# Kernel optimization log

Hardware: AMD Instinct MI355X
Metric: run time of the kernel (lower is better)

## Reference

```python
import jax, jax.numpy as jnp
import numpy as np

SIZE = 128
N_ATOMS = 100000
N_BONDS = 400000
N_PAIRS = 400000
N_ANGLES = 800000
LN_EPS = 1e-5


def _layernorm(h, w, b):
    m = jnp.mean(h, axis=-1, keepdims=True)
    v = jnp.mean(jnp.square(h - m), axis=-1, keepdims=True)
    return (h - m) * jax.lax.rsqrt(v + LN_EPS) * w + b


def _forward(x, bond_x, sc_pair_x, angles,
             W_bm, W_sc, W1, b1, W2, b2,
             ln1_w, ln1_b, ln2_w, ln2_b,
             bond_idx, sc_idx, angles_idx):
    n_atoms = x.shape[0]
    n_bonds = bond_x.shape[0]

    # ---- sublayer 1: bond message passing ----
    h = _layernorm(x, ln1_w, ln1_b)                       # [n_atoms, d]
    # aggregate angle features onto bonds
    bond_ang = jax.ops.segment_sum(angles, angles_idx, num_segments=n_bonds)
    src, dst = bond_idx[:, 0], bond_idx[:, 1]
    msg = jax.nn.relu((h[src] + bond_x + bond_ang) @ W_bm)  # [n_bonds, d]
    agg = jax.ops.segment_sum(msg, dst, num_segments=n_atoms)
    x = x + (agg @ W1 + b1)                               # residual (dropout=0)

    # ---- sublayer 2: scalar-coupling pair message passing ----
    h2 = _layernorm(x, ln2_w, ln2_b)
    i, j = sc_idx[:, 0], sc_idx[:, 1]
    msg2 = jax.nn.relu((h2[i] + h2[j] + sc_pair_x) @ W_sc)  # [n_pairs, d]
    agg2 = jax.ops.segment_sum(msg2, i, num_segments=n_atoms)
    return x + (agg2 @ W2 + b2)


def setup_inputs() -> dict:
    key = jax.random.key(0)
    ks = jax.random.split(key, 16)
    s = 1.0 / np.sqrt(SIZE)
    inp = {
        "x": jax.random.normal(ks[0], (N_ATOMS, SIZE), jnp.float32),
        "bond_x": jax.random.normal(ks[1], (N_BONDS, SIZE), jnp.float32),
        "sc_pair_x": jax.random.normal(ks[2], (N_PAIRS, SIZE), jnp.float32),
        "angles": jax.random.normal(ks[3], (N_ANGLES, SIZE), jnp.float32),
        "W_bm": jax.random.normal(ks[4], (SIZE, SIZE), jnp.float32) * s,
        "W_sc": jax.random.normal(ks[5], (SIZE, SIZE), jnp.float32) * s,
        "W1": jax.random.normal(ks[6], (SIZE, SIZE), jnp.float32) * s,
        "b1": jnp.zeros((SIZE,), jnp.float32),
        "W2": jax.random.normal(ks[7], (SIZE, SIZE), jnp.float32) * s,
        "b2": jnp.zeros((SIZE,), jnp.float32),
        "ln1_w": jax.random.uniform(ks[8], (SIZE,), jnp.float32),
        "ln1_b": jnp.zeros((SIZE,), jnp.float32),
        "ln2_w": jax.random.uniform(ks[9], (SIZE,), jnp.float32),
        "ln2_b": jnp.zeros((SIZE,), jnp.float32),
        "mask": jnp.ones((N_ATOMS,), jnp.bool_),
        "bond_idx": jax.random.randint(ks[10], (N_BONDS, 2), 0, N_ATOMS),
        "sc_idx": jax.random.randint(ks[11], (N_PAIRS, 2), 0, N_ATOMS),
        "angles_idx": jax.random.randint(ks[12], (N_ANGLES,), 0, N_BONDS),
    }
    return inp


def reference(x, bond_x, sc_pair_x, angles, W_bm, W_sc, W1, b1, W2, b2,
              ln1_w, ln1_b, ln2_w, ln2_b, mask, bond_idx, sc_idx, angles_idx):
    # mask is in the torch forward signature but unused in its body
    return _forward(x, bond_x, sc_pair_x, angles, W_bm, W_sc, W1, b1, W2, b2,
                    ln1_w, ln1_b, ln2_w, ln2_b, bond_idx, sc_idx, angles_idx)
```

## Files before the change

### kernel.cpp

```cpp
#include <hip/hip_runtime.h>

#define SZ 128
#define NATOMS 100000
#define NBONDS 400000
#define NPAIRS 400000
#define NANG   800000

typedef float f32x4 __attribute__((ext_vector_type(4)));
typedef short s16x8 __attribute__((ext_vector_type(8)));

__device__ __forceinline__ unsigned short f2bf(float f) {
  union { float f; unsigned u; } v; v.f = f;
  unsigned r = v.u + 0x7FFFu + ((v.u >> 16) & 1u);
  return (unsigned short)(r >> 16);
}
__device__ __forceinline__ float bf2f(unsigned short h) {
  union { unsigned u; float f; } v; v.u = ((unsigned)h) << 16;
  return v.f;
}

#define AGG_OFF      0ull
#define AGG2_OFF     51200000ull
#define CNT_OFF      102400000ull
#define FILL_OFF     104000000ull
#define ZERO_BYTES   105600000ull
#define START_OFF    105600000ull
#define ALIST_OFF    107200000ull
#define BSUM_OFF     110400000ull
#define H_OFF        110404096ull
#define H2_OFF       136004096ull
#define WT_BM_OFF    161604096ull
#define WT_SC_OFF    (WT_BM_OFF + 32768ull)
#define WT1_OFF      (WT_SC_OFF + 32768ull)
#define WT2_OFF      (WT1_OFF + 32768ull)

#define SCAN_EPB 1024
#define NSCAN_BLOCKS ((NBONDS + SCAN_EPB - 1) / SCAN_EPB)

__global__ __launch_bounds__(256) void k_prep_w(const float* __restrict__ W,
                                                s16x8* __restrict__ Wt) {
  int cid = blockIdx.x * 256 + threadIdx.x;
  int nt8 = cid >> 8, kk = (cid >> 6) & 3, l = cid & 63;
  int col = nt8 * 16 + (l & 15);
  int k0  = kk * 32 + (l >> 4) * 8;
  s16x8 v;
#pragma unroll
  for (int i = 0; i < 8; ++i) v[i] = (short)f2bf(W[(k0 + i) * SZ + col]);
  Wt[cid] = v;
}

__global__ __launch_bounds__(256) void k_ln(const float* __restrict__ x,
                                            const float* __restrict__ g,
                                            const float* __restrict__ bvec,
                                            unsigned short* __restrict__ hout) {
  int row  = blockIdx.x * 4 + (threadIdx.x >> 6);
  int lane = threadIdx.x & 63;
  float2 v = *(const float2*)(x + (size_t)row * SZ + lane * 2);
  float s = v.x + v.y, sq = v.x * v.x + v.y * v.y;
#pragma unroll
  for (int off = 32; off; off >>= 1) { s += __shfl_xor(s, off); sq += __shfl_xor(sq, off); }
  float m = s * 0.0078125f;
  float var = sq * 0.0078125f - m * m;
  float rstd = rsqrtf(var + 1e-5f);
  float2 gv = *(const float2*)(g + lane * 2);
  float2 bv = *(const float2*)(bvec + lane * 2);
  float y0 = (v.x - m) * rstd * gv.x + bv.x;
  float y1 = (v.y - m) * rstd * gv.y + bv.y;
  unsigned pack = (unsigned)f2bf(y0) | ((unsigned)f2bf(y1) << 16);
  ((unsigned*)hout)[(size_t)row * 64 + lane] = pack;
}

__global__ __launch_bounds__(256) void k_hist(const int* __restrict__ aidx,
                                              int* __restrict__ cnt) {
  int id = blockIdx.x * 256 + threadIdx.x;
  if (id < NANG) atomicAdd(&cnt[aidx[id]], 1);
}

__global__ __launch_bounds__(256) void k_scan1(const int* __restrict__ cnt,
                                               int* __restrict__ start,
                                               int* __restrict__ bsum) {
  __shared__ int wsum[4];
  int tid = threadIdx.x, bid = blockIdx.x;
  int base = bid * SCAN_EPB + tid * 4;
  int4 c;
  if (base + 3 < NBONDS) {
    c = *(const int4*)(cnt + base);
  } else {
    c.x = (base + 0 < NBONDS) ? cnt[base + 0] : 0;
    c.y = (base + 1 < NBONDS) ? cnt[base + 1] : 0;
    c.z = (base + 2 < NBONDS) ? cnt[base + 2] : 0;
    c.w = (base + 3 < NBONDS) ? cnt[base + 3] : 0;
  }
  int tsum = c.x + c.y + c.z + c.w;
  int lane = tid & 63, wid = tid >> 6;
  int inc = tsum;
#pragma unroll
  for (int off = 1; off < 64; off <<= 1) {
    int o = __shfl_up(inc, off);
    if (lane >= off) inc += o;
  }
  if (lane == 63) wsum[wid] = inc;
  __syncthreads();
  int woff = 0;
#pragma unroll
  for (int wq = 0; wq < 4; ++wq) { if (wq < wid) woff += wsum[wq]; }
  int s0 = woff + inc - tsum;
  if (base + 0 < NBONDS) { start[base + 0] = s0; } s0 += c.x;
  if (base + 1 < NBONDS) { start[base + 1] = s0; } s0 += c.y;
  if (base + 2 < NBONDS) { start[base + 2] = s0; } s0 += c.z;
  if (base + 3 < NBONDS) { start[base + 3] = s0; }
  if (tid == 255) {
    int tot = 0;
#pragma unroll
    for (int wq = 0; wq < 4; ++wq) tot += wsum[wq];
    bsum[bid] = tot;
  }
}

__global__ __launch_bounds__(512) void k_scan2(int* __restrict__ bsum, int n) {
  __shared__ int tmp[2][512];
  int tid = threadIdx.x;
  tmp[0][tid] = (tid < n) ? bsum[tid] : 0;
  int pi = 0;
  for (int off = 1; off < 512; off <<= 1) {
    __syncthreads();
    int t = tmp[pi][tid];
    if (tid >= off) t += tmp[pi][tid - off];
    tmp[pi ^ 1][tid] = t;
    pi ^= 1;
  }
  __syncthreads();
  if (tid < n) bsum[tid] = (tid == 0) ? 0 : tmp[pi][tid - 1];
}

__global__ __launch_bounds__(256) void k_scan_add(int* __restrict__ start,
                                                  const int* __restrict__ bsum) {
  int id = blockIdx.x * 256 + threadIdx.x;
  if (id < NBONDS) start[id] += bsum[id / SCAN_EPB];
}

__global__ __launch_bounds__(256) void k_fill(const int* __restrict__ aidx,
                                              const int* __restrict__ start,
                                              int* __restrict__ fill,
                                              int* __restrict__ alist) {
  int id = blockIdx.x * 256 + threadIdx.x;
  if (id < NANG) {
    int b = aidx[id];
    int p = atomicAdd(&fill[b], 1);
    alist[start[b] + p] = id;
  }
}

__global__ __launch_bounds__(256, 4) void k_msg1(const unsigned short* __restrict__ h,
                                                 const float* __restrict__ bx,
                                                 const float* __restrict__ angles,
                                                 const int* __restrict__ start,
                                                 const int* __restrict__ cnt,
                                                 const int* __restrict__ alist,
                                                 const int* __restrict__ bidx,
                                                 const s16x8* __restrict__ Wt,
                                                 float* __restrict__ agg) {
  __shared__ s16x8 Wl[2048];
  int tid = threadIdx.x;
  for (int i = tid; i < 2048; i += 256) Wl[i] = Wt[i];
  __syncthreads();
  int w = tid >> 6, l = tid & 63;
  int grp = l >> 4;
  int rl  = l & 15;
  int gw = blockIdx.x * 4 + w;
  int nw = gridDim.x * 4;
  for (int tile = gw; tile < NBONDS / 16; tile += nw) {
    int base = tile * 16;
    int b = base + rl;
    int s = bidx[2 * b];
    int s0 = start[b], nc = cnt[b];
    int aj[4] = {0, 0, 0, 0};
#pragma unroll
    for (int t = 0; t < 4; ++t) {
      if (t < nc) aj[t] = alist[s0 + t];
    }
    f32x4 acc[8];
#pragma unroll
    for (int nb = 0; nb < 8; ++nb) acc[nb] = (f32x4){0.f, 0.f, 0.f, 0.f};
#pragma unroll
    for (int kk = 0; kk < 4; ++kk) {
      const int co = kk * 32 + grp * 8;
      uint4 hv = *(const uint4*)(h + (size_t)s * SZ + co);
      float4 b0 = *(const float4*)(bx + (size_t)b * SZ + co);
      float4 b1 = *(const float4*)(bx + (size_t)b * SZ + co + 4);
      float a[8];
      a[0] = b0.x; a[1] = b0.y; a[2] = b0.z; a[3] = b0.w;
      a[4] = b1.x; a[5] = b1.y; a[6] = b1.z; a[7] = b1.w;
#pragma unroll
      for (int t = 0; t < 4; ++t) {
        if (t < nc) {
          const float* ap = angles + (size_t)aj[t] * SZ + co;
          float4 u0 = *(const float4*)ap;
          float4 u1 = *(const float4*)(ap + 4);
          a[0] += u0.x; a[1] += u0.y; a[2] += u0.z; a[3] += u0.w;
          a[4] += u1.x; a[5] += u1.y; a[6] += u1.z; a[7] += u1.w;
        }
      }
      for (int t = 4; t < nc; ++t) {
        int ar = alist[s0 + t];
        const float* ap = angles + (size_t)ar * SZ + co;
        float4 u0 = *(const float4*)ap;
        float4 u1 = *(const float4*)(ap + 4);
        a[0] += u0.x; a[1] += u0.y; a[2] += u0.z; a[3] += u0.w;
        a[4] += u1.x; a[5] += u1.y; a[6] += u1.z; a[7] += u1.w;
      }
      const unsigned short* hp = (const unsigned short*)&hv;
      s16x8 af;
#pragma unroll
      for (int i = 0; i < 8; ++i) af[i] = (short)f2bf(bf2f(hp[i]) + a[i]);
#pragma unroll
      for (int nb = 0; nb < 8; ++nb)
        acc[nb] = __builtin_amdgcn_mfma_f32_16x16x32_bf16(af, Wl[(nb * 4 + kk) * 64 + l], acc[nb], 0, 0, 0);
    }
#pragma unroll
    for (int p = 0; p < 4; ++p) {
      int row = base + grp * 4 + p;
      int d = bidx[2 * row + 1];
      float* pb = agg + (size_t)d * SZ + rl;
#pragma unroll
      for (int nb = 0; nb < 8; ++nb)
        unsafeAtomicAdd(pb + nb * 16, fmaxf(acc[nb][p], 0.f));
    }
  }
}

__global__ __launch_bounds__(256, 4) void k_msg2(const unsigned short* __restrict__ h2,
                                                 const float* __restrict__ scp,
                                                 const int* __restrict__ sidx,
                                                 const s16x8* __restrict__ Wt,
                                                 float* __restrict__ agg2) {
  __shared__ s16x8 Wl[2048];
  int tid = threadIdx.x;
  for (int i = tid; i < 2048; i += 256) Wl[i] = Wt[i];
  __syncthreads();
  int w = tid >> 6, l = tid & 63;
  int grp = l >> 4;
  int rl  = l & 15;
  int gw = blockIdx.x * 4 + w;
  int nw = gridDim.x * 4;
  for (int tile = gw; tile < NPAIRS / 16; tile += nw) {
    int base = tile * 16;
    int b = base + rl;
    int i0 = sidx[2 * b], j0 = sidx[2 * b + 1];
    f32x4 acc[8];
#pragma unroll
    for (int nb = 0; nb < 8; ++nb) acc[nb] = (f32x4){0.f, 0.f, 0.f, 0.f};
#pragma unroll
    for (int kk = 0; kk < 4; ++kk) {
      const int co = kk * 32 + grp * 8;
      uint4 hv1 = *(const uint4*)(h2 + (size_t)i0 * SZ + co);
      uint4 hv2 = *(const uint4*)(h2 + (size_t)j0 * SZ + co);
      float4 s0v = *(const float4*)(scp + (size_t)b * SZ + co);
      float4 s1v = *(const float4*)(scp + (size_t)b * SZ + co + 4);
      const unsigned short* p1 = (const unsigned short*)&hv1;
      const unsigned short* p2 = (const unsigned short*)&hv2;
      float a[8];
      a[0] = s0v.x; a[1] = s0v.y; a[2] = s0v.z; a[3] = s0v.w;
      a[4] = s1v.x; a[5] = s1v.y; a[6] = s1v.z; a[7] = s1v.w;
      s16x8 af;
#pragma unroll
      for (int i = 0; i < 8; ++i) af[i] = (short)f2bf(bf2f(p1[i]) + bf2f(p2[i]) + a[i]);
#pragma unroll
      for (int nb = 0; nb < 8; ++nb)
        acc[nb] = __builtin_amdgcn_mfma_f32_16x16x32_bf16(af, Wl[(nb * 4 + kk) * 64 + l], acc[nb], 0, 0, 0);
    }
#pragma unroll
    for (int p = 0; p < 4; ++p) {
      int row = base + grp * 4 + p;
      int d = sidx[2 * row];
      float* pb = agg2 + (size_t)d * SZ + rl;
#pragma unroll
      for (int nb = 0; nb < 8; ++nb)
        unsafeAtomicAdd(pb + nb * 16, fmaxf(acc[nb][p], 0.f));
    }
  }
}

__global__ __launch_bounds__(256) void k_update1(const float* __restrict__ agg,
                                                 const float* __restrict__ x,
                                                 const float* __restrict__ b1,
                                                 const float* __restrict__ lnw,
                                                 const float* __restrict__ lnb,
                                                 const s16x8* __restrict__ Wt,
                                                 float* __restrict__ out,
                                                 unsigned short* __restrict__ h2) {
  __shared__ s16x8 Wl[2048];
  __shared__ s16x8 Tl[256];
  __shared__ float Xl[16][128];
  int tid = threadIdx.x;
  for (int i = tid; i < 2048; i += 256) Wl[i] = Wt[i];
  __syncthreads();
  int r = tid >> 4, kc = tid & 15;
  int w = tid >> 6, l = tid & 63;
  int colb = w * 32 + (l & 15);
  int rowb = (l >> 4) * 4;
  float bb0 = b1[colb], bb1 = b1[colb + 16];
  float2 g2 = *(const float2*)(lnw + l * 2);
  float2 be2 = *(const float2*)(lnb + l * 2);
  for (int tile = blockIdx.x; tile < NATOMS / 16; tile += gridDim.x) {
    int base = tile * 16;
    int a = base + r;
    float qb[8];
    *(float4*)&qb[0] = *(const float4*)(agg + (size_t)a * SZ + kc * 8);
    *(float4*)&qb[4] = *(const float4*)(agg + (size_t)a * SZ + kc * 8 + 4);
    s16x8 tv;
#pragma unroll
    for (int i = 0; i < 8; ++i) tv[i] = (short)f2bf(qb[i]);
    Tl[(kc >> 2) * 64 + (kc & 3) * 16 + r] = tv;
    __syncthreads();
    f32x4 acc0 = {0.f, 0.f, 0.f, 0.f}, acc1 = {0.f, 0.f, 0.f, 0.f};
#pragma unroll
    for (int kk = 0; kk < 4; ++kk) {
      s16x8 av = Tl[kk * 64 + l];
      acc0 = __builtin_amdgcn_mfma_f32_16x16x32_bf16(av, Wl[((w * 2 + 0) * 4 + kk) * 64 + l], acc0, 0, 0, 0);
      acc1 = __builtin_amdgcn_mfma_f32_16x16x32_bf16(av, Wl[((w * 2 + 1) * 4 + kk) * 64 + l], acc1, 0, 0, 0);
    }
#pragma unroll
    for (int p = 0; p < 4; ++p) {
      int atom = base + rowb + p;
      float v0 = acc0[p] + bb0 + x[(size_t)atom * SZ + colb];
      float v1 = acc1[p] + bb1 + x[(size_t)atom * SZ + colb + 16];
      out[(size_t)atom * SZ + colb] = v0;
      out[(size_t)atom * SZ + colb + 16] = v1;
      Xl[rowb + p][colb] = v0;
      Xl[rowb + p][colb + 16] = v1;
    }
    __syncthreads();
#pragma unroll
    for (int rr = 0; rr < 4; ++rr) {
      int rw = w * 4 + rr;
      float2 v = *(const float2*)&Xl[rw][l * 2];
      float s = v.x + v.y, sq = v.x * v.x + v.y * v.y;
#pragma unroll
      for (int off = 32; off; off >>= 1) { s += __shfl_xor(s, off); sq += __shfl_xor(sq, off); }
      float m = s * 0.0078125f;
      float var = sq * 0.0078125f - m * m;
      float rstd = rsqrtf(var + 1e-5f);
      float y0 = (v.x - m) * rstd * g2.x + be2.x;
      float y1 = (v.y - m) * rstd * g2.y + be2.y;
      unsigned pack = (unsigned)f2bf(y0) | ((unsigned)f2bf(y1) << 16);
      ((unsigned*)h2)[(size_t)(base + rw) * 64 + l] = pack;
    }
    __syncthreads();
  }
}

__global__ __launch_bounds__(256) void k_update2(const float* __restrict__ agg2,
                                                 const float* __restrict__ b2,
                                                 const s16x8* __restrict__ Wt,
                                                 float* __restrict__ out) {
  __shared__ s16x8 Wl[2048];
  __shared__ s16x8 Tl[256];
  int tid = threadIdx.x;
  for (int i = tid; i < 2048; i += 256) Wl[i] = Wt[i];
  __syncthreads();
  int r = tid >> 4, kc = tid & 15;
  int w = tid >> 6, l = tid & 63;
  int colb = w * 32 + (l & 15);
  int rowb = (l >> 4) * 4;
  float bb0 = b2[colb], bb1 = b2[colb + 16];
  for (int tile = blockIdx.x; tile < NATOMS / 16; tile += gridDim.x) {
    int base = tile * 16;
    int a = base + r;
    float qb[8];
    *(float4*)&qb[0] = *(const float4*)(agg2 + (size_t)a * SZ + kc * 8);
    *(float4*)&qb[4] = *(const float4*)(agg2 + (size_t)a * SZ + kc * 8 + 4);
    s16x8 tv;
#pragma unroll
    for (int i = 0; i < 8; ++i) tv[i] = (short)f2bf(qb[i]);
    Tl[(kc >> 2) * 64 + (kc & 3) * 16 + r] = tv;
    __syncthreads();
    f32x4 acc0 = {0.f, 0.f, 0.f, 0.f}, acc1 = {0.f, 0.f, 0.f, 0.f};
#pragma unroll
    for (int kk = 0; kk < 4; ++kk) {
      s16x8 av = Tl[kk * 64 + l];
      acc0 = __builtin_amdgcn_mfma_f32_16x16x32_bf16(av, Wl[((w * 2 + 0) * 4 + kk) * 64 + l], acc0, 0, 0, 0);
      acc1 = __builtin_amdgcn_mfma_f32_16x16x32_bf16(av, Wl[((w * 2 + 1) * 4 + kk) * 64 + l], acc1, 0, 0, 0);
    }
#pragma unroll
    for (int p = 0; p < 4; ++p) {
      int atom = base + rowb + p;
      out[(size_t)atom * SZ + colb]      += acc0[p] + bb0;
      out[(size_t)atom * SZ + colb + 16] += acc1[p] + bb1;
    }
    __syncthreads();
  }
}

extern "C" void kernel_launch(void* const* d_in, const int* in_sizes, int n_in,
                              void* d_out, int out_size, void* d_ws, size_t ws_size,
                              hipStream_t stream) {
  (void)in_sizes; (void)n_in; (void)out_size; (void)ws_size;
  const float* x        = (const float*)d_in[0];
  const float* bond_x   = (const float*)d_in[1];
  const float* sc_pair  = (const float*)d_in[2];
  const float* angles   = (const float*)d_in[3];
  const float* W_bm     = (const float*)d_in[4];
  const float* W_sc     = (const float*)d_in[5];
  const float* W1       = (const float*)d_in[6];
  const float* b1       = (const float*)d_in[7];
  const float* W2       = (const float*)d_in[8];
  const float* b2       = (const float*)d_in[9];
  const float* ln1w     = (const float*)d_in[10];
  const float* ln1b     = (const float*)d_in[11];
  const float* ln2w     = (const float*)d_in[12];
  const float* ln2b     = (const float*)d_in[13];
  const int* bond_idx   = (const int*)d_in[15];
  const int* sc_idx     = (const int*)d_in[16];
  const int* ang_idx    = (const int*)d_in[17];
  float* out = (float*)d_out;
  char* ws = (char*)d_ws;

  float* agg      = (float*)(ws + AGG_OFF);
  float* agg2     = (float*)(ws + AGG2_OFF);
  int*   cnt      = (int*)(ws + CNT_OFF);
  int*   fill     = (int*)(ws + FILL_OFF);
  int*   start    = (int*)(ws + START_OFF);
  int*   alist    = (int*)(ws + ALIST_OFF);
  int*   bsum     = (int*)(ws + BSUM_OFF);
  unsigned short* hbuf  = (unsigned short*)(ws + H_OFF);
  unsigned short* h2buf = (unsigned short*)(ws + H2_OFF);
  s16x8* wt_bm = (s16x8*)(ws + WT_BM_OFF);
  s16x8* wt_sc = (s16x8*)(ws + WT_SC_OFF);
  s16x8* wt1   = (s16x8*)(ws + WT1_OFF);
  s16x8* wt2   = (s16x8*)(ws + WT2_OFF);

  hipMemsetAsync(ws, 0, ZERO_BYTES, stream);

  k_prep_w<<<8, 256, 0, stream>>>(W_bm, wt_bm);
  k_prep_w<<<8, 256, 0, stream>>>(W_sc, wt_sc);
  k_prep_w<<<8, 256, 0, stream>>>(W1, wt1);
  k_prep_w<<<8, 256, 0, stream>>>(W2, wt2);

  k_hist<<<(NANG + 255) / 256, 256, 0, stream>>>(ang_idx, cnt);
  k_scan1<<<NSCAN_BLOCKS, 256, 0, stream>>>(cnt, start, bsum);
  k_scan2<<<1, 512, 0, stream>>>(bsum, NSCAN_BLOCKS);
  k_scan_add<<<(NBONDS + 255) / 256, 256, 0, stream>>>(start, bsum);
  k_fill<<<(NANG + 255) / 256, 256, 0, stream>>>(ang_idx, start, fill, alist);

  k_ln<<<NATOMS / 4, 256, 0, stream>>>(x, ln1w, ln1b, hbuf);
  k_msg1<<<2048, 256, 0, stream>>>(hbuf, bond_x, angles, start, cnt, alist, bond_idx, wt_bm, agg);
  k_update1<<<1024, 256, 0, stream>>>(agg, x, b1, ln2w, ln2b, wt1, out, h2buf);
  k_msg2<<<2048, 256, 0, stream>>>(h2buf, sc_pair, sc_idx, wt_sc, agg2);
  k_update2<<<1024, 256, 0, stream>>>(agg2, b2, wt2, out);
}
```

Measured before the change: 795.0 us.

## Sort bonds and pairs by destination atom and merge same-target atomics

Builds counting-sort permutations of bonds (by destination atom) and pairs (by source atom i), then processes edges in that sorted order in the message kernels. Consecutive rows with the same destination are summed in registers before a single atomic add, which cuts the number of global float atomics and improves their locality. In exchange it adds ten extra small prep kernels and makes the bond_x and sc_pair_x row gathers indirect, so those reads are no longer contiguous. With random indices and about four edges per atom, adjacent rows in a group of four often share a destination.

```diff
diff --git a/kernel.cpp b/kernel.cpp
--- a/kernel.cpp
+++ b/kernel.cpp
@@ -23,19 +23,30 @@
 #define AGG2_OFF     51200000ull
 #define CNT_OFF      102400000ull
 #define FILL_OFF     104000000ull
-#define ZERO_BYTES   105600000ull
-#define START_OFF    105600000ull
-#define ALIST_OFF    107200000ull
-#define BSUM_OFF     110400000ull
-#define H_OFF        110404096ull
-#define H2_OFF       136004096ull
-#define WT_BM_OFF    161604096ull
+#define CNTB_OFF     105600000ull
+#define FILLB_OFF    106000000ull
+#define CNTP_OFF     106400000ull
+#define FILLP_OFF    106800000ull
+#define ZERO_BYTES   107200000ull
+#define START_OFF    107200000ull
+#define ALIST_OFF    108800000ull
+#define BSUM_OFF     112000000ull
+#define STARTB_OFF   112004096ull
+#define BLIST_OFF    112404096ull
+#define DLIST_OFF    114004096ull
+#define BSUMB_OFF    115604096ull
+#define STARTP_OFF   115608192ull
+#define PLIST_OFF    116008192ull
+#define ILIST_OFF    117608192ull
+#define BSUMP_OFF    119208192ull
+#define H_OFF        119212288ull
+#define H2_OFF       144812288ull
+#define WT_BM_OFF    170412288ull
 #define WT_SC_OFF    (WT_BM_OFF + 32768ull)
 #define WT1_OFF      (WT_SC_OFF + 32768ull)
 #define WT2_OFF      (WT1_OFF + 32768ull)
 
 #define SCAN_EPB 1024
-#define NSCAN_BLOCKS ((NBONDS + SCAN_EPB - 1) / SCAN_EPB)
 
 __global__ __launch_bounds__(256) void k_prep_w(const float* __restrict__ W,
                                                 s16x8* __restrict__ Wt) {
@@ -70,26 +81,27 @@
   ((unsigned*)hout)[(size_t)row * 64 + lane] = pack;
 }
 
-__global__ __launch_bounds__(256) void k_hist(const int* __restrict__ aidx,
+__global__ __launch_bounds__(256) void k_hist(const int* __restrict__ idx, int n,
+                                              int stride, int off,
                                               int* __restrict__ cnt) {
   int id = blockIdx.x * 256 + threadIdx.x;
-  if (id < NANG) atomicAdd(&cnt[aidx[id]], 1);
+  if (id < n) atomicAdd(&cnt[idx[id * stride + off]], 1);
 }
 
 __global__ __launch_bounds__(256) void k_scan1(const int* __restrict__ cnt,
                                                int* __restrict__ start,
-                                               int* __restrict__ bsum) {
+                                               int* __restrict__ bsum, int N) {
   __shared__ int wsum[4];
   int tid = threadIdx.x, bid = blockIdx.x;
   int base = bid * SCAN_EPB + tid * 4;
   int4 c;
-  if (base + 3 < NBONDS) {
+  if (base + 3 < N) {
     c = *(const int4*)(cnt + base);
   } else {
-    c.x = (base + 0 < NBONDS) ? cnt[base + 0] : 0;
-    c.y = (base + 1 < NBONDS) ? cnt[base + 1] : 0;
-    c.z = (base + 2 < NBONDS) ? cnt[base + 2] : 0;
-    c.w = (base + 3 < NBONDS) ? cnt[base + 3] : 0;
+    c.x = (base + 0 < N) ? cnt[base + 0] : 0;
+    c.y = (base + 1 < N) ? cnt[base + 1] : 0;
+    c.z = (base + 2 < N) ? cnt[base + 2] : 0;
+    c.w = (base + 3 < N) ? cnt[base + 3] : 0;
   }
   int tsum = c.x + c.y + c.z + c.w;
   int lane = tid & 63, wid = tid >> 6;
@@ -105,10 +117,10 @@
 #pragma unroll
   for (int wq = 0; wq < 4; ++wq) { if (wq < wid) woff += wsum[wq]; }
   int s0 = woff + inc - tsum;
-  if (base + 0 < NBONDS) { start[base + 0] = s0; } s0 += c.x;
-  if (base + 1 < NBONDS) { start[base + 1] = s0; } s0 += c.y;
-  if (base + 2 < NBONDS) { start[base + 2] = s0; } s0 += c.z;
-  if (base + 3 < NBONDS) { start[base + 3] = s0; }
+  if (base + 0 < N) { start[base + 0] = s0; } s0 += c.x;
+  if (base + 1 < N) { start[base + 1] = s0; } s0 += c.y;
+  if (base + 2 < N) { start[base + 2] = s0; } s0 += c.z;
+  if (base + 3 < N) { start[base + 3] = s0; }
   if (tid == 255) {
     int tot = 0;
 #pragma unroll
@@ -134,20 +146,24 @@
 }
 
 __global__ __launch_bounds__(256) void k_scan_add(int* __restrict__ start,
-                                                  const int* __restrict__ bsum) {
+                                                  const int* __restrict__ bsum, int N) {
   int id = blockIdx.x * 256 + threadIdx.x;
-  if (id < NBONDS) start[id] += bsum[id / SCAN_EPB];
-}
-
-__global__ __launch_bounds__(256) void k_fill(const int* __restrict__ aidx,
+  if (id < N) start[id] += bsum[id / SCAN_EPB];
+}
+
+__global__ __launch_bounds__(256) void k_fill(const int* __restrict__ idx, int n,
+                                              int stride, int off,
                                               const int* __restrict__ start,
                                               int* __restrict__ fill,
-                                              int* __restrict__ alist) {
+                                              int* __restrict__ list,
+                                              int* __restrict__ klist) {
   int id = blockIdx.x * 256 + threadIdx.x;
-  if (id < NANG) {
-    int b = aidx[id];
-    int p = atomicAdd(&fill[b], 1);
-    alist[start[b] + p] = id;
+  if (id < n) {
+    int k = idx[id * stride + off];
+    int p = atomicAdd(&fill[k], 1);
+    int pos = start[k] + p;
+    list[pos] = id;
+    if (klist) klist[pos] = k;
   }
 }
 
@@ -158,6 +174,8 @@
                                                  const int* __restrict__ cnt,
                                                  const int* __restrict__ alist,
                                                  const int* __restrict__ bidx,
+                                                 const int* __restrict__ blist,
+                                                 const int* __restrict__ dlist,
                                                  const s16x8* __restrict__ Wt,
                                                  float* __restrict__ agg) {
   __shared__ s16x8 Wl[2048];
@@ -171,7 +189,7 @@
   int nw = gridDim.x * 4;
   for (int tile = gw; tile < NBONDS / 16; tile += nw) {
     int base = tile * 16;
-    int b = base + rl;
+    int b = blist[base + rl];
     int s = bidx[2 * b];
     int s0 = start[b], nc = cnt[b];
     int aj[4] = {0, 0, 0, 0};
@@ -217,21 +235,37 @@
       for (int nb = 0; nb < 8; ++nb)
         acc[nb] = __builtin_amdgcn_mfma_f32_16x16x32_bf16(af, Wl[(nb * 4 + kk) * 64 + l], acc[nb], 0, 0, 0);
     }
-#pragma unroll
-    for (int p = 0; p < 4; ++p) {
-      int row = base + grp * 4 + p;
-      int d = bidx[2 * row + 1];
-      float* pb = agg + (size_t)d * SZ + rl;
-#pragma unroll
-      for (int nb = 0; nb < 8; ++nb)
-        unsafeAtomicAdd(pb + nb * 16, fmaxf(acc[nb][p], 0.f));
-    }
+    int4 dv = *(const int4*)(dlist + base + grp * 4);
+    int dn[4] = {dv.x, dv.y, dv.z, dv.w};
+    float v[8];
+#pragma unroll
+    for (int nb = 0; nb < 8; ++nb) v[nb] = fmaxf(acc[nb][0], 0.f);
+    int dprev = dn[0];
+#pragma unroll
+    for (int p = 1; p < 4; ++p) {
+      if (dn[p] == dprev) {
+#pragma unroll
+        for (int nb = 0; nb < 8; ++nb) v[nb] += fmaxf(acc[nb][p], 0.f);
+      } else {
+        float* pb = agg + (size_t)dprev * SZ + rl;
+#pragma unroll
+        for (int nb = 0; nb < 8; ++nb) unsafeAtomicAdd(pb + nb * 16, v[nb]);
+#pragma unroll
+        for (int nb = 0; nb < 8; ++nb) v[nb] = fmaxf(acc[nb][p], 0.f);
+        dprev = dn[p];
+      }
+    }
+    float* pb = agg + (size_t)dprev * SZ + rl;
+#pragma unroll
+    for (int nb = 0; nb < 8; ++nb) unsafeAtomicAdd(pb + nb * 16, v[nb]);
   }
 }
 
 __global__ __launch_bounds__(256, 4) void k_msg2(const unsigned short* __restrict__ h2,
                                                  const float* __restrict__ scp,
                                                  const int* __restrict__ sidx,
+                                                 const int* __restrict__ plist,
+                                                 const int* __restrict__ ilist,
                                                  const s16x8* __restrict__ Wt,
                                                  float* __restrict__ agg2) {
   __shared__ s16x8 Wl[2048];
@@ -245,8 +279,9 @@
   int nw = gridDim.x * 4;
   for (int tile = gw; tile < NPAIRS / 16; tile += nw) {
     int base = tile * 16;
-    int b = base + rl;
-    int i0 = sidx[2 * b], j0 = sidx[2 * b + 1];
+    int b = plist[base + rl];
+    int i0 = ilist[base + rl];
+    int j0 = sidx[2 * b + 1];
     f32x4 acc[8];
 #pragma unroll
     for (int nb = 0; nb < 8; ++nb) acc[nb] = (f32x4){0.f, 0.f, 0.f, 0.f};
@@ -269,15 +304,29 @@
       for (int nb = 0; nb < 8; ++nb)
         acc[nb] = __builtin_amdgcn_mfma_f32_16x16x32_bf16(af, Wl[(nb * 4 + kk) * 64 + l], acc[nb], 0, 0, 0);
     }
-#pragma unroll
-    for (int p = 0; p < 4; ++p) {
-      int row = base + grp * 4 + p;
-      int d = sidx[2 * row];
-      float* pb = agg2 + (size_t)d * SZ + rl;
-#pragma unroll
-      for (int nb = 0; nb < 8; ++nb)
-        unsafeAtomicAdd(pb + nb * 16, fmaxf(acc[nb][p], 0.f));
-    }
+    int4 dv = *(const int4*)(ilist + base + grp * 4);
+    int dn[4] = {dv.x, dv.y, dv.z, dv.w};
+    float v[8];
+#pragma unroll
+    for (int nb = 0; nb < 8; ++nb) v[nb] = fmaxf(acc[nb][0], 0.f);
+    int dprev = dn[0];
+#pragma unroll
+    for (int p = 1; p < 4; ++p) {
+      if (dn[p] == dprev) {
+#pragma unroll
+        for (int nb = 0; nb < 8; ++nb) v[nb] += fmaxf(acc[nb][p], 0.f);
+      } else {
+        float* pb = agg2 + (size_t)dprev * SZ + rl;
+#pragma unroll
+        for (int nb = 0; nb < 8; ++nb) unsafeAtomicAdd(pb + nb * 16, v[nb]);
+#pragma unroll
+        for (int nb = 0; nb < 8; ++nb) v[nb] = fmaxf(acc[nb][p], 0.f);
+        dprev = dn[p];
+      }
+    }
+    float* pb = agg2 + (size_t)dprev * SZ + rl;
+#pragma unroll
+    for (int nb = 0; nb < 8; ++nb) unsafeAtomicAdd(pb + nb * 16, v[nb]);
   }
 }
 
@@ -420,9 +469,21 @@
   float* agg2     = (float*)(ws + AGG2_OFF);
   int*   cnt      = (int*)(ws + CNT_OFF);
   int*   fill     = (int*)(ws + FILL_OFF);
+  int*   cntb     = (int*)(ws + CNTB_OFF);
+  int*   fillb    = (int*)(ws + FILLB_OFF);
+  int*   cntp     = (int*)(ws + CNTP_OFF);
+  int*   fillp    = (int*)(ws + FILLP_OFF);
   int*   start    = (int*)(ws + START_OFF);
   int*   alist    = (int*)(ws + ALIST_OFF);
   int*   bsum     = (int*)(ws + BSUM_OFF);
+  int*   startb   = (int*)(ws + STARTB_OFF);
+  int*   blist    = (int*)(ws + BLIST_OFF);
+  int*   dlist    = (int*)(ws + DLIST_OFF);
+  int*   bsumb    = (int*)(ws + BSUMB_OFF);
+  int*   startp   = (int*)(ws + STARTP_OFF);
+  int*   plist    = (int*)(ws + PLIST_OFF);
+  int*   ilist    = (int*)(ws + ILIST_OFF);
+  int*   bsump    = (int*)(ws + BSUMP_OFF);
   unsigned short* hbuf  = (unsigned short*)(ws + H_OFF);
   unsigned short* h2buf = (unsigned short*)(ws + H2_OFF);
   s16x8* wt_bm = (s16x8*)(ws + WT_BM_OFF);
@@ -437,15 +498,30 @@
   k_prep_w<<<8, 256, 0, stream>>>(W1, wt1);
   k_prep_w<<<8, 256, 0, stream>>>(W2, wt2);
 
-  k_hist<<<(NANG + 255) / 256, 256, 0, stream>>>(ang_idx, cnt);
-  k_scan1<<<NSCAN_BLOCKS, 256, 0, stream>>>(cnt, start, bsum);
-  k_scan2<<<1, 512, 0, stream>>>(bsum, NSCAN_BLOCKS);
-  k_scan_add<<<(NBONDS + 255) / 256, 256, 0, stream>>>(start, bsum);
-  k_fill<<<(NANG + 255) / 256, 256, 0, stream>>>(ang_idx, start, fill, alist);
+  const int NSB_ANG  = (NBONDS + SCAN_EPB - 1) / SCAN_EPB;
+  const int NSB_ATOM = (NATOMS + SCAN_EPB - 1) / SCAN_EPB;
+
+  k_hist<<<(NANG + 255) / 256, 256, 0, stream>>>(ang_idx, NANG, 1, 0, cnt);
+  k_scan1<<<NSB_ANG, 256, 0, stream>>>(cnt, start, bsum, NBONDS);
+  k_scan2<<<1, 512, 0, stream>>>(bsum, NSB_ANG);
+  k_scan_add<<<(NBONDS + 255) / 256, 256, 0, stream>>>(start, bsum, NBONDS);
+  k_fill<<<(NANG + 255) / 256, 256, 0, stream>>>(ang_idx, NANG, 1, 0, start, fill, alist, (int*)nullptr);
+
+  k_hist<<<(NBONDS + 255) / 256, 256, 0, stream>>>(bond_idx, NBONDS, 2, 1, cntb);
+  k_scan1<<<NSB_ATOM, 256, 0, stream>>>(cntb, startb, bsumb, NATOMS);
+  k_scan2<<<1, 512, 0, stream>>>(bsumb, NSB_ATOM);
+  k_scan_add<<<(NATOMS + 255) / 256, 256, 0, stream>>>(startb, bsumb, NATOMS);
+  k_fill<<<(NBONDS + 255) / 256, 256, 0, stream>>>(bond_idx, NBONDS, 2, 1, startb, fillb, blist, dlist);
+
+  k_hist<<<(NPAIRS + 255) / 256, 256, 0, stream>>>(sc_idx, NPAIRS, 2, 0, cntp);
+  k_scan1<<<NSB_ATOM, 256, 0, stream>>>(cntp, startp, bsump, NATOMS);
+  k_scan2<<<1, 512, 0, stream>>>(bsump, NSB_ATOM);
+  k_scan_add<<<(NATOMS + 255) / 256, 256, 0, stream>>>(startp, bsump, NATOMS);
+  k_fill<<<(NPAIRS + 255) / 256, 256, 0, stream>>>(sc_idx, NPAIRS, 2, 0, startp, fillp, plist, ilist);
 
   k_ln<<<NATOMS / 4, 256, 0, stream>>>(x, ln1w, ln1b, hbuf);
-  k_msg1<<<2048, 256, 0, stream>>>(hbuf, bond_x, angles, start, cnt, alist, bond_idx, wt_bm, agg);
+  k_msg1<<<2048, 256, 0, stream>>>(hbuf, bond_x, angles, start, cnt, alist, bond_idx, blist, dlist, wt_bm, agg);
   k_update1<<<1024, 256, 0, stream>>>(agg, x, b1, ln2w, ln2b, wt1, out, h2buf);
-  k_msg2<<<2048, 256, 0, stream>>>(h2buf, sc_pair, sc_idx, wt_sc, agg2);
+  k_msg2<<<2048, 256, 0, stream>>>(h2buf, sc_pair, sc_idx, plist, ilist, wt_sc, agg2);
   k_update2<<<1024, 256, 0, stream>>>(agg2, b2, wt2, out);
 }
```

New measurement: 836.2 us. 5.2% more time.
